# Optimization experiments

Hardware: AMD Instinct MI355X
Metric: run time of the kernel (lower is better)

Reference implementation:

```python
import jax, jax.numpy as jnp
import numpy as np

B, T, D, H = 4, 1024, 1024, 16
TP = 1024
HD = D // H
LN_EPS = 1e-3  # keras LayerNormalization default epsilon


def snac_linear(x, wt, mt):
    # conv1dsnac: w = tanh(wt) * sigmoid(mt), shape [1, nx, nf] -> [nx, nf]
    w = (jnp.tanh(wt) * jax.nn.sigmoid(mt))[0]
    return jnp.einsum('btx,xf->btf', x, w)


def layernorm(x, gamma, beta):
    mu = jnp.mean(x, axis=-1, keepdims=True)
    var = jnp.mean(jnp.square(x - mu), axis=-1, keepdims=True)
    return (x - mu) * jax.lax.rsqrt(var + LN_EPS) * gamma + beta


def setup_inputs() -> dict:
    key = jax.random.key(0)
    ks = jax.random.split(key, 10)
    s = 0.02
    return {
        'input': jax.random.normal(ks[0], (B, T, D), jnp.float32),
        'past': jax.random.normal(ks[1], (B, 2, H, TP, HD), jnp.float32),
        'qkv_wt': jax.random.normal(ks[2], (1, D, 3 * D), jnp.float32) * s,
        'qkv_mt': jax.random.normal(ks[3], (1, D, 3 * D), jnp.float32) * s,
        'merge_wt': jax.random.normal(ks[4], (1, D, D), jnp.float32) * s,
        'merge_mt': jax.random.normal(ks[5], (1, D, D), jnp.float32) * s,
        'ln1_wt': jax.random.normal(ks[6], (1, D, D), jnp.float32) * s,
        'ln1_mt': jax.random.normal(ks[7], (1, D, D), jnp.float32) * s,
        'g1': jnp.ones((D,), jnp.float32), 'b1': jnp.zeros((D,), jnp.float32),
        'g2': jnp.ones((D,), jnp.float32), 'b2': jnp.zeros((D,), jnp.float32),
    }


def reference(input, past, qkv_wt, qkv_mt, merge_wt, merge_mt, ln1_wt, ln1_mt, g1, b1, g2, b2):
    x = input
    xn = layernorm(x, g1, b1)
    c = snac_linear(xn, qkv_wt, qkv_mt)  # [B, T, 3D]
    q, k, v = jnp.split(c, 3, axis=2)
    # split heads -> [B, H, T, HD]
    to_heads = lambda t: t.reshape(B, T, H, HD).transpose(0, 2, 1, 3)
    q, k, v = to_heads(q), to_heads(k), to_heads(v)
    present = jnp.stack([k, v], axis=1)  # [B, 2, H, T, HD]
    pk, pv = past[:, 0], past[:, 1]
    k = jnp.concatenate([pk, k], axis=2)  # [B, H, TP+T, HD]
    v = jnp.concatenate([pv, v], axis=2)
    nd, ns = T, TP + T
    w = jnp.einsum('bhqd,bhkd->bhqk', q, k) * jax.lax.rsqrt(jnp.float32(HD))
    i = jnp.arange(nd)[:, None]
    j = jnp.arange(ns)[None, :]
    m = (i >= j - ns + nd).astype(w.dtype)  # [nd, ns] causal mask incl. past
    w = w * m - jnp.asarray(1e10, w.dtype) * (1 - m)
    msk = jax.nn.softmax(w, axis=-1)  # [B, H, T, TP+T]
    a = jnp.einsum('bhqk,bhkd->bhqd', msk, v)
    ah = a.transpose(0, 2, 1, 3).reshape(B, T, D)  # merge heads
    am = snac_linear(ah, merge_wt, merge_mt)
    xa = x + am
    mlp = snac_linear(layernorm(xa, g2, b2), ln1_wt, ln1_mt)
    xm = xa + mlp
    return xm, present, msk
```

## Files before the change

kernel.cpp:

```cpp
#include <hip/hip_runtime.h>
#include <hip/hip_bf16.h>

typedef _Float16 half8 __attribute__((ext_vector_type(8)));
typedef _Float16 half4v __attribute__((ext_vector_type(4)));
typedef float f32x4 __attribute__((ext_vector_type(4)));

#define DEV static __device__ __forceinline__


typedef __attribute__((address_space(1))) const unsigned int* gas_p;
typedef __attribute__((address_space(3))) unsigned int* las_p;
DEV void glds16(const void* g, void* s) {
  __builtin_amdgcn_global_load_lds((gas_p)g, (las_p)s, 16, 0, 0);
}

__global__ __launch_bounds__(256) void prep_w(const float* __restrict__ wt,
                                              const float* __restrict__ mt,
                                              _Float16* __restrict__ out, int N) {
  __shared__ float tile[64][65];
  const int ntiles = N >> 6;
  const int nt = blockIdx.x % ntiles, kt = blockIdx.x / ntiles;
  const int k0 = kt << 6, n0 = nt << 6;
  const int t = threadIdx.x, r = t >> 2, c0 = (t & 3) << 4;
  const long ibase = (long)(k0 + r) * N + n0 + c0;
#pragma unroll
  for (int j = 0; j < 16; j += 4) {
    float4 a = *(const float4*)(wt + ibase + j);
    float4 b = *(const float4*)(mt + ibase + j);
    tile[r][c0 + j + 0] = tanhf(a.x) / (1.f + __expf(-b.x));
    tile[r][c0 + j + 1] = tanhf(a.y) / (1.f + __expf(-b.y));
    tile[r][c0 + j + 2] = tanhf(a.z) / (1.f + __expf(-b.z));
    tile[r][c0 + j + 3] = tanhf(a.w) / (1.f + __expf(-b.w));
  }
  __syncthreads();
  half8 o0, o1;
#pragma unroll
  for (int j = 0; j < 8; ++j) {
    o0[j] = (_Float16)tile[c0 + j][r];
    o1[j] = (_Float16)tile[c0 + 8 + j][r];
  }
  _Float16* dst = out + (long)(n0 + r) * 1024 + k0 + c0;
  *(half8*)dst = o0;
  *(half8*)(dst + 8) = o1;
}

__global__ __launch_bounds__(256) void conv_pastk(const float* __restrict__ past,
                                                  _Float16* __restrict__ kf) {
  const long e = ((long)blockIdx.x * 256 + threadIdx.x) * 4;
  const int b = (int)(e >> 20);
  const int rem = (int)(e & 1048575);
  float4 v = *(const float4*)(past + (long)b * 2097152 + rem);
  half4v o = {(_Float16)v.x, (_Float16)v.y, (_Float16)v.z, (_Float16)v.w};
  const int h = rem >> 16, td = rem & 65535;
  *(half4v*)(kf + (long)(b * 16 + h) * 131072 + td) = o;
}

__global__ __launch_bounds__(256) void ln_k(const float* __restrict__ x,
                                            const float* __restrict__ g,
                                            const float* __restrict__ be,
                                            _Float16* __restrict__ out) {
  __shared__ float red[4];
  const int row = blockIdx.x, tid = threadIdx.x, l = tid & 63, w = tid >> 6;
  float4 v = *(const float4*)(x + (long)row * 1024 + tid * 4);
  float s = v.x + v.y + v.z + v.w;
#pragma unroll
  for (int o = 32; o > 0; o >>= 1) s += __shfl_down(s, o, 64);
  if (l == 0) red[w] = s;
  __syncthreads();
  const float mu = (red[0] + red[1] + red[2] + red[3]) * (1.f / 1024.f);
  float dx = v.x - mu, dy = v.y - mu, dz = v.z - mu, dw = v.w - mu;
  float ss = dx * dx + dy * dy + dz * dz + dw * dw;
#pragma unroll
  for (int o = 32; o > 0; o >>= 1) ss += __shfl_down(ss, o, 64);
  __syncthreads();
  if (l == 0) red[w] = ss;
  __syncthreads();
  const float var = (red[0] + red[1] + red[2] + red[3]) * (1.f / 1024.f);
  const float rs = rsqrtf(var + 1e-3f);
  float4 gv = *(const float4*)(g + tid * 4);
  float4 bv = *(const float4*)(be + tid * 4);
  half4v o = {(_Float16)(dx * rs * gv.x + bv.x), (_Float16)(dy * rs * gv.y + bv.y),
              (_Float16)(dz * rs * gv.z + bv.z), (_Float16)(dw * rs * gv.w + bv.w)};
  *(half4v*)(out + (long)row * 1024 + tid * 4) = o;
}

template <int BM, int EPI>
__global__ __launch_bounds__(256) void gemm_k(const _Float16* __restrict__ A,
                                              const _Float16* __restrict__ Bt,
                                              int mtiles,
                                              _Float16* __restrict__ e_q,
                                              _Float16* __restrict__ e_k,
                                              _Float16* __restrict__ e_v,
                                              float* __restrict__ e_present,
                                              const float* __restrict__ e_res,
                                              float* __restrict__ e_out) {
  constexpr int FM = BM / 32;
  __shared__ __align__(16) char smem[2 * BM * 128 + 32768];
  char* Bbase = smem + 2 * BM * 128;
  const int tid = threadIdx.x, l = tid & 63, w = tid >> 6;
  const int wm = w >> 1, wn = w & 1;
  const int bm = blockIdx.x % mtiles, bn = blockIdx.x / mtiles;
  const long m0 = (long)bm * BM, n0 = (long)bn * 128;

  f32x4 acc[FM][4];
#pragma unroll
  for (int i = 0; i < FM; ++i)
#pragma unroll
    for (int j = 0; j < 4; ++j) acc[i][j] = (f32x4){0.f, 0.f, 0.f, 0.f};

  auto stage = [&](int b, int kt) {
#pragma unroll
    for (int i = 0; i < FM; ++i) {
      const int cid = i * 256 + tid, row = cid >> 3, u = cid & 7;
      glds16(A + (m0 + row) * 1024 + kt * 64 + ((u ^ (row & 7)) << 3),
             smem + b * BM * 128 + i * 4096 + w * 1024);
    }
#pragma unroll
    for (int i = 0; i < 4; ++i) {
      const int cid = i * 256 + tid, row = cid >> 3, u = cid & 7;
      glds16(Bt + (n0 + row) * 1024 + kt * 64 + ((u ^ (row & 7)) << 3),
             Bbase + b * 16384 + i * 4096 + w * 1024);
    }
  };

  stage(0, 0);
  __syncthreads();
  for (int kt = 0; kt < 16; ++kt) {
    const int cur = kt & 1;
    if (kt < 15) stage(cur ^ 1, kt + 1);
    const char* As = smem + cur * BM * 128;
    const char* Bs = Bbase + cur * 16384;
#pragma unroll
    for (int k2 = 0; k2 < 2; ++k2) {
      const int sl = k2 * 4 + (l >> 4);
      half8 bfr[4];
#pragma unroll
      for (int fn = 0; fn < 4; ++fn) {
        const int rn = wn * 64 + fn * 16 + (l & 15);
        bfr[fn] = *(const half8*)(Bs + rn * 128 + ((sl ^ (rn & 7)) << 4));
      }
#pragma unroll
      for (int fm = 0; fm < FM; ++fm) {
        const int rm = wm * (BM / 2) + fm * 16 + (l & 15);
        const half8 afr = *(const half8*)(As + rm * 128 + ((sl ^ (rm & 7)) << 4));
#pragma unroll
        for (int fn = 0; fn < 4; ++fn)
          acc[fm][fn] = __builtin_amdgcn_mfma_f32_16x16x32_f16(afr, bfr[fn], acc[fm][fn], 0, 0, 0);
      }
    }
    __syncthreads();
  }
#pragma unroll
  for (int fm = 0; fm < FM; ++fm) {
#pragma unroll
    for (int fn = 0; fn < 4; ++fn) {
#pragma unroll
      for (int r = 0; r < 4; ++r) {
        const long row = m0 + wm * (BM / 2) + fm * 16 + (l >> 4) * 4 + r;
        const long col = n0 + fn * 16 + (l & 15) + wn * 64;
        const float v = acc[fm][fn][r];
        if constexpr (EPI == 0) {
          const int b = (int)(row >> 10), t = (int)(row & 1023);
          const int sec = (int)(col >> 10), h = ((int)col >> 6) & 15, hd = (int)col & 63;
          const long bh = b * 16 + h;
          if (sec == 0) {
            e_q[(bh * 1024 + t) * 64 + hd] = (_Float16)v;
          } else if (sec == 1) {
            e_present[(((long)(b * 2) * 16 + h) * 1024 + t) * 64 + hd] = v;
            e_k[(bh * 2048 + 1024 + t) * 64 + hd] = (_Float16)v;
          } else {
            e_present[(((long)(b * 2 + 1) * 16 + h) * 1024 + t) * 64 + hd] = v;
            e_v[(bh * 1024 + t) * 64 + hd] = (_Float16)v;
          }
        } else {
          e_out[row * 1024 + col] = e_res[row * 1024 + col] + v;
        }
      }
    }
  }
}

__global__ __launch_bounds__(256) void vt_transpose(const float* __restrict__ past,
                                                    const _Float16* __restrict__ vnew,
                                                    _Float16* __restrict__ vt) {
  __shared__ float tile[64][65];
  const int bh = blockIdx.x >> 5, kt = blockIdx.x & 31;
  const int b = bh >> 4, h = bh & 15;
  const int k0 = kt << 6;
  const int t = threadIdx.x, r = t >> 2, c0 = (t & 3) << 4;
  if (k0 < 1024) {
    const float* src = past + (((long)(b * 2 + 1) * 16 + h) * 1024 + (k0 + r)) * 64 + c0;
#pragma unroll
    for (int j = 0; j < 16; j += 4) {
      float4 v = *(const float4*)(src + j);
      tile[r][c0 + j + 0] = v.x;
      tile[r][c0 + j + 1] = v.y;
      tile[r][c0 + j + 2] = v.z;
      tile[r][c0 + j + 3] = v.w;
    }
  } else {
    const _Float16* src = vnew + ((long)bh * 1024 + (k0 - 1024 + r)) * 64 + c0;
    half8 a = *(const half8*)src;
    half8 bq = *(const half8*)(src + 8);
#pragma unroll
    for (int j = 0; j < 8; ++j) {
      tile[r][c0 + j] = (float)a[j];
      tile[r][c0 + 8 + j] = (float)bq[j];
    }
  }
  __syncthreads();
  half8 o0, o1;
#pragma unroll
  for (int j = 0; j < 8; ++j) {
    o0[j] = (_Float16)tile[c0 + j][r];
    o1[j] = (_Float16)tile[c0 + 8 + j][r];
  }
  _Float16* dst = vt + ((long)bh * 64 + r) * 2048 + k0 + c0;
  *(half8*)dst = o0;
  *(half8*)(dst + 8) = o1;
}

__global__ __launch_bounds__(256, 2) void attn_k(const _Float16* __restrict__ qg,
                                                 const _Float16* __restrict__ kg,
                                                 const _Float16* __restrict__ vtg,
                                                 float* __restrict__ msk,
                                                 _Float16* __restrict__ ah) {
  __shared__ __align__(16) char smem[81920];
  char* ps_all = smem + 65536;
  const int tid = threadIdx.x, l = tid & 63, w = tid >> 6;
  char* psw = ps_all + w * 4096;
  const int lq = l & 15, hi = l >> 4;

  const int x = blockIdx.x & 7, g = blockIdx.x >> 3;
  const int bh = (g & 7) * 8 + x;
  const int qt = 15 - (g >> 3);
  const int r0 = qt << 6;
  const int nc = (r0 + 1215) >> 7;
  const int rowg0 = r0 + w * 16;

  const _Float16* kb = kg + (long)bh * 131072;
  const _Float16* vb = vtg + (long)bh * 131072;
  float* mskb = msk + ((long)bh * 1024 + rowg0) * 2048;

  half8 qa[2];
  {
    const _Float16* qp = qg + ((long)bh * 1024 + rowg0 + lq) * 64 + hi * 8;
    qa[0] = *(const half8*)qp;
    qa[1] = *(const half8*)(qp + 32);
  }

  auto stageK = [&](int b, int c) {
#pragma unroll
    for (int i = 0; i < 4; ++i) {
      const int cid = i * 256 + tid, row = cid >> 3, u = cid & 7;
      glds16(kb + (long)(c * 128 + row) * 64 + ((u ^ (row & 7)) << 3),
             smem + b * 32768 + i * 4096 + w * 1024);
    }
  };
  auto stageV = [&](int b, int c) {
#pragma unroll
    for (int i = 0; i < 4; ++i) {
      const int cid = i * 256 + tid, row = cid >> 4, u = cid & 15;
      glds16(vb + (long)row * 2048 + c * 128 + ((u ^ (row & 7)) << 3),
             smem + b * 32768 + 16384 + i * 4096 + w * 1024);
    }
  };

  constexpr float C1 = 0.125f * 1.44269504088896341f;

  auto qk_tile = [&](const char* ks, f32x4 (&sa)[8]) {
#pragma unroll
    for (int fn = 0; fn < 8; ++fn) sa[fn] = (f32x4){0.f, 0.f, 0.f, 0.f};
#pragma unroll
    for (int k2 = 0; k2 < 2; ++k2) {
      const int sl = k2 * 4 + hi;
      half8 ak[8];
#pragma unroll
      for (int fn = 0; fn < 8; ++fn) {
        const int rn = fn * 16 + lq;
        ak[fn] = *(const half8*)(ks + rn * 128 + ((sl ^ (rn & 7)) << 4));
      }
#pragma unroll
      for (int fn = 0; fn < 8; ++fn)
        sa[fn] = __builtin_amdgcn_mfma_f32_16x16x32_f16(ak[fn], qa[k2], sa[fn], 0, 0, 0);
    }
  };

  const int lim = rowg0 + lq + 1024;

  float rsum = 0.f;
  stageK(0, 0);
  __syncthreads();
  for (int c = 0; c < nc; ++c) {
    const int cur = c & 1;
    if (c + 1 < nc) stageK(cur ^ 1, c + 1);
    f32x4 sa[8];
    qk_tile(smem + cur * 32768, sa);
    if (c < nc - 1) {
#pragma unroll
      for (int fn = 0; fn < 8; ++fn)
#pragma unroll
        for (int r = 0; r < 4; ++r) rsum += __builtin_amdgcn_exp2f(sa[fn][r] * C1);
    } else {
#pragma unroll
      for (int fn = 0; fn < 8; ++fn)
#pragma unroll
        for (int r = 0; r < 4; ++r) {
          const int col = c * 128 + fn * 16 + hi * 4 + r;
          const float e = __builtin_amdgcn_exp2f(sa[fn][r] * C1);
          rsum += (col <= lim) ? e : 0.f;
        }
    }
    __syncthreads();
  }
  rsum += __shfl_xor(rsum, 16, 64);
  rsum += __shfl_xor(rsum, 32, 64);
  const float c2s = -__builtin_amdgcn_logf(rsum);

  f32x4 pv[4];
#pragma unroll
  for (int j = 0; j < 4; ++j) pv[j] = (f32x4){0.f, 0.f, 0.f, 0.f};
  stageK(0, 0);
  stageV(0, 0);
  __syncthreads();
  for (int c = 0; c < nc; ++c) {
    const int cur = c & 1;
    if (c + 1 < nc) {
      stageK(cur ^ 1, c + 1);
      stageV(cur ^ 1, c + 1);
    }
    f32x4 sa[8];
    qk_tile(smem + cur * 32768, sa);
    const bool bound = (c == nc - 1);
#pragma unroll
    for (int fn = 0; fn < 8; ++fn) {
      float pr[4];
#pragma unroll
      for (int r = 0; r < 4; ++r) {
        float p = __builtin_amdgcn_exp2f(sa[fn][r] * C1 + c2s);
        if (bound) {
          const int col = c * 128 + fn * 16 + hi * 4 + r;
          p = (col <= lim) ? p : 0.f;
        }
        pr[r] = p;
      }
      *(float4*)(mskb + (long)lq * 2048 + c * 128 + fn * 16 + hi * 4) =
          make_float4(pr[0], pr[1], pr[2], pr[3]);
      const half4v hv = {(_Float16)pr[0], (_Float16)pr[1], (_Float16)pr[2],
                         (_Float16)pr[3]};
      const int bc = fn * 32 + hi * 8;
      *(half4v*)(psw + lq * 256 + ((((bc >> 4) ^ (lq & 7)) << 4) | (bc & 15))) = hv;
    }
    __builtin_amdgcn_wave_barrier();
    asm volatile("s_waitcnt lgkmcnt(0)" ::: "memory");
    __builtin_amdgcn_sched_barrier(0);
    const char* vs = smem + cur * 32768 + 16384;
#pragma unroll
    for (int k2p = 0; k2p < 4; ++k2p) {
      const int sl2 = k2p * 4 + hi;
      const half8 pa = *(const half8*)(psw + lq * 256 + ((sl2 ^ (lq & 7)) << 4));
      half8 bv[4];
#pragma unroll
      for (int fn2 = 0; fn2 < 4; ++fn2) {
        const int rd = fn2 * 16 + lq;
        bv[fn2] = *(const half8*)(vs + rd * 256 + ((sl2 ^ (rd & 7)) << 4));
      }
#pragma unroll
      for (int fn2 = 0; fn2 < 4; ++fn2)
        pv[fn2] = __builtin_amdgcn_mfma_f32_16x16x32_f16(pa, bv[fn2], pv[fn2], 0, 0, 0);
    }
    __syncthreads();
  }

  const int ntail = (16 - nc) << 5;
  if (ntail > 0) {
    const float4 z4 = make_float4(0.f, 0.f, 0.f, 0.f);
    for (int row = 0; row < 16; ++row)
      for (int i = l; i < ntail; i += 64)
        *(float4*)(mskb + (long)row * 2048 + nc * 128 + i * 4) = z4;
  }

  const int b_ = bh >> 4, h_ = bh & 15;
  _Float16* ahb = ah + ((long)b_ * 1024 + rowg0) * 1024 + h_ * 64;
#pragma unroll
  for (int fn2 = 0; fn2 < 4; ++fn2)
#pragma unroll
    for (int r = 0; r < 4; ++r)
      ahb[(long)(hi * 4 + r) * 1024 + fn2 * 16 + lq] = (_Float16)pv[fn2][r];
}

extern "C" void kernel_launch(void* const* d_in, const int* in_sizes, int n_in,
                              void* d_out, int out_size, void* d_ws, size_t ws_size,
                              hipStream_t stream) {
  const float* x = (const float*)d_in[0];
  const float* past = (const float*)d_in[1];
  const float* qkv_wt = (const float*)d_in[2];
  const float* qkv_mt = (const float*)d_in[3];
  const float* merge_wt = (const float*)d_in[4];
  const float* merge_mt = (const float*)d_in[5];
  const float* ln1_wt = (const float*)d_in[6];
  const float* ln1_mt = (const float*)d_in[7];
  const float* g1 = (const float*)d_in[8];
  const float* b1 = (const float*)d_in[9];
  const float* g2 = (const float*)d_in[10];
  const float* b2 = (const float*)d_in[11];

  float* out = (float*)d_out;
  float* o_xm = out;
  float* o_present = out + 4194304;
  float* o_msk = out + 4194304 + 8388608;

  char* ws = (char*)d_ws;
  _Float16* wq_t = (_Float16*)(ws + 0);
  _Float16* wm_t = (_Float16*)(ws + 6291456);
  _Float16* wl_t = (_Float16*)(ws + 8388608);
  _Float16* xn   = (_Float16*)(ws + 10485760);
  _Float16* qws  = (_Float16*)(ws + 18874368);
  _Float16* kful = (_Float16*)(ws + 27262976);
  _Float16* vnew = (_Float16*)(ws + 44040192);
  _Float16* vt   = (_Float16*)(ws + 52428800);
  _Float16* ah   = (_Float16*)(ws + 69206016);
  float* xa      = (float*)(ws + 77594624);

  prep_w<<<768, 256, 0, stream>>>(qkv_wt, qkv_mt, wq_t, 3072);
  prep_w<<<256, 256, 0, stream>>>(merge_wt, merge_mt, wm_t, 1024);
  prep_w<<<256, 256, 0, stream>>>(ln1_wt, ln1_mt, wl_t, 1024);
  conv_pastk<<<4096, 256, 0, stream>>>(past, kful);
  ln_k<<<4096, 256, 0, stream>>>(x, g1, b1, xn);
  gemm_k<128, 0><<<768, 256, 0, stream>>>(xn, wq_t, 32, qws, kful, vnew, o_present,
                                          nullptr, nullptr);
  vt_transpose<<<2048, 256, 0, stream>>>(past, vnew, vt);
  attn_k<<<1024, 256, 0, stream>>>(qws, kful, vt, o_msk, ah);
  gemm_k<64, 1><<<512, 256, 0, stream>>>(ah, wm_t, 64, nullptr, nullptr, nullptr,
                                         nullptr, x, xa);
  ln_k<<<4096, 256, 0, stream>>>(xa, g2, b2, xn);
  gemm_k<64, 1><<<512, 256, 0, stream>>>(xn, wl_t, 64, nullptr, nullptr, nullptr,
                                         nullptr, xa, o_xm);
}
```

Before: 302.7 us.

## Read K and V directly from global, shrink LDS, raise occupancy, nontemporal mask stores

The first softmax-denominator pass now loads K fragments straight from global memory into registers instead of staging them through double-buffered LDS with block barriers. The second pass no longer stages V in LDS and reads V^T fragments directly from global. Together these cut LDS use from 80KB to 48KB so launch bounds can request 3 blocks per CU. The large fp32 mask output is written with nontemporal stores to avoid polluting cache. The trade-off is more uncoalesced global and L2 traffic for K and V and higher register pressure under the tighter occupancy bound.

```diff
diff --git a/kernel.cpp b/kernel.cpp
--- a/kernel.cpp
+++ b/kernel.cpp
@@ -12,6 +12,9 @@
 typedef __attribute__((address_space(3))) unsigned int* las_p;
 DEV void glds16(const void* g, void* s) {
   __builtin_amdgcn_global_load_lds((gas_p)g, (las_p)s, 16, 0, 0);
+}
+DEV void nt_store4(float* p, f32x4 v) {
+  __builtin_nontemporal_store(v, (f32x4*)p);
 }
 
 __global__ __launch_bounds__(256) void prep_w(const float* __restrict__ wt,
@@ -220,13 +223,13 @@
   *(half8*)(dst + 8) = o1;
 }
 
-__global__ __launch_bounds__(256, 2) void attn_k(const _Float16* __restrict__ qg,
+__global__ __launch_bounds__(256, 3) void attn_k(const _Float16* __restrict__ qg,
                                                  const _Float16* __restrict__ kg,
                                                  const _Float16* __restrict__ vtg,
                                                  float* __restrict__ msk,
                                                  _Float16* __restrict__ ah) {
-  __shared__ __align__(16) char smem[81920];
-  char* ps_all = smem + 65536;
+  __shared__ __align__(16) char smem[49152];
+  char* ps_all = smem + 32768;
   const int tid = threadIdx.x, l = tid & 63, w = tid >> 6;
   char* psw = ps_all + w * 4096;
   const int lq = l & 15, hi = l >> 4;
@@ -254,48 +257,30 @@
     for (int i = 0; i < 4; ++i) {
       const int cid = i * 256 + tid, row = cid >> 3, u = cid & 7;
       glds16(kb + (long)(c * 128 + row) * 64 + ((u ^ (row & 7)) << 3),
-             smem + b * 32768 + i * 4096 + w * 1024);
+             smem + b * 16384 + i * 4096 + w * 1024);
     }
   };
-  auto stageV = [&](int b, int c) {
-#pragma unroll
-    for (int i = 0; i < 4; ++i) {
-      const int cid = i * 256 + tid, row = cid >> 4, u = cid & 15;
-      glds16(vb + (long)row * 2048 + c * 128 + ((u ^ (row & 7)) << 3),
-             smem + b * 32768 + 16384 + i * 4096 + w * 1024);
-    }
-  };
 
   constexpr float C1 = 0.125f * 1.44269504088896341f;
-
-  auto qk_tile = [&](const char* ks, f32x4 (&sa)[8]) {
+  const int lim = rowg0 + lq + 1024;
+
+  float rsum = 0.f;
+  for (int c = 0; c < nc; ++c) {
+    half8 ak[2][8];
+#pragma unroll
+    for (int k2 = 0; k2 < 2; ++k2)
+#pragma unroll
+      for (int fn = 0; fn < 8; ++fn)
+        ak[k2][fn] = *(const half8*)(kb + (long)(c * 128 + fn * 16 + lq) * 64 +
+                                     k2 * 32 + hi * 8);
+    f32x4 sa[8];
 #pragma unroll
     for (int fn = 0; fn < 8; ++fn) sa[fn] = (f32x4){0.f, 0.f, 0.f, 0.f};
 #pragma unroll
-    for (int k2 = 0; k2 < 2; ++k2) {
-      const int sl = k2 * 4 + hi;
-      half8 ak[8];
-#pragma unroll
-      for (int fn = 0; fn < 8; ++fn) {
-        const int rn = fn * 16 + lq;
-        ak[fn] = *(const half8*)(ks + rn * 128 + ((sl ^ (rn & 7)) << 4));
-      }
+    for (int k2 = 0; k2 < 2; ++k2)
 #pragma unroll
       for (int fn = 0; fn < 8; ++fn)
-        sa[fn] = __builtin_amdgcn_mfma_f32_16x16x32_f16(ak[fn], qa[k2], sa[fn], 0, 0, 0);
-    }
-  };
-
-  const int lim = rowg0 + lq + 1024;
-
-  float rsum = 0.f;
-  stageK(0, 0);
-  __syncthreads();
-  for (int c = 0; c < nc; ++c) {
-    const int cur = c & 1;
-    if (c + 1 < nc) stageK(cur ^ 1, c + 1);
-    f32x4 sa[8];
-    qk_tile(smem + cur * 32768, sa);
+        sa[fn] = __builtin_amdgcn_mfma_f32_16x16x32_f16(ak[k2][fn], qa[k2], sa[fn], 0, 0, 0);
     if (c < nc - 1) {
 #pragma unroll
       for (int fn = 0; fn < 8; ++fn)
@@ -311,26 +296,39 @@
           rsum += (col <= lim) ? e : 0.f;
         }
     }
-    __syncthreads();
   }
   rsum += __shfl_xor(rsum, 16, 64);
   rsum += __shfl_xor(rsum, 32, 64);
   const float c2s = -__builtin_amdgcn_logf(rsum);
 
+  auto qk_tile = [&](const char* ks, f32x4 (&sa)[8]) {
+#pragma unroll
+    for (int fn = 0; fn < 8; ++fn) sa[fn] = (f32x4){0.f, 0.f, 0.f, 0.f};
+#pragma unroll
+    for (int k2 = 0; k2 < 2; ++k2) {
+      const int sl = k2 * 4 + hi;
+      half8 ak[8];
+#pragma unroll
+      for (int fn = 0; fn < 8; ++fn) {
+        const int rn = fn * 16 + lq;
+        ak[fn] = *(const half8*)(ks + rn * 128 + ((sl ^ (rn & 7)) << 4));
+      }
+#pragma unroll
+      for (int fn = 0; fn < 8; ++fn)
+        sa[fn] = __builtin_amdgcn_mfma_f32_16x16x32_f16(ak[fn], qa[k2], sa[fn], 0, 0, 0);
+    }
+  };
+
   f32x4 pv[4];
 #pragma unroll
   for (int j = 0; j < 4; ++j) pv[j] = (f32x4){0.f, 0.f, 0.f, 0.f};
   stageK(0, 0);
-  stageV(0, 0);
   __syncthreads();
   for (int c = 0; c < nc; ++c) {
     const int cur = c & 1;
-    if (c + 1 < nc) {
-      stageK(cur ^ 1, c + 1);
-      stageV(cur ^ 1, c + 1);
-    }
+    if (c + 1 < nc) stageK(cur ^ 1, c + 1);
     f32x4 sa[8];
-    qk_tile(smem + cur * 32768, sa);
+    qk_tile(smem + cur * 16384, sa);
     const bool bound = (c == nc - 1);
 #pragma unroll
     for (int fn = 0; fn < 8; ++fn) {
@@ -344,8 +342,8 @@
         }
         pr[r] = p;
       }
-      *(float4*)(mskb + (long)lq * 2048 + c * 128 + fn * 16 + hi * 4) =
-          make_float4(pr[0], pr[1], pr[2], pr[3]);
+      nt_store4(mskb + (long)lq * 2048 + c * 128 + fn * 16 + hi * 4,
+                (f32x4){pr[0], pr[1], pr[2], pr[3]});
       const half4v hv = {(_Float16)pr[0], (_Float16)pr[1], (_Float16)pr[2],
                          (_Float16)pr[3]};
       const int bc = fn * 32 + hi * 8;
@@ -354,17 +352,14 @@
     __builtin_amdgcn_wave_barrier();
     asm volatile("s_waitcnt lgkmcnt(0)" ::: "memory");
     __builtin_amdgcn_sched_barrier(0);
-    const char* vs = smem + cur * 32768 + 16384;
 #pragma unroll
     for (int k2p = 0; k2p < 4; ++k2p) {
       const int sl2 = k2p * 4 + hi;
       const half8 pa = *(const half8*)(psw + lq * 256 + ((sl2 ^ (lq & 7)) << 4));
       half8 bv[4];
 #pragma unroll
-      for (int fn2 = 0; fn2 < 4; ++fn2) {
-        const int rd = fn2 * 16 + lq;
-        bv[fn2] = *(const half8*)(vs + rd * 256 + ((sl2 ^ (rd & 7)) << 4));
-      }
+      for (int fn2 = 0; fn2 < 4; ++fn2)
+        bv[fn2] = *(const half8*)(vb + (long)(fn2 * 16 + lq) * 2048 + c * 128 + sl2 * 8);
 #pragma unroll
       for (int fn2 = 0; fn2 < 4; ++fn2)
         pv[fn2] = __builtin_amdgcn_mfma_f32_16x16x32_f16(pa, bv[fn2], pv[fn2], 0, 0, 0);
@@ -374,10 +369,10 @@
 
   const int ntail = (16 - nc) << 5;
   if (ntail > 0) {
-    const float4 z4 = make_float4(0.f, 0.f, 0.f, 0.f);
     for (int row = 0; row < 16; ++row)
       for (int i = l; i < ntail; i += 64)
-        *(float4*)(mskb + (long)row * 2048 + nc * 128 + i * 4) = z4;
+        nt_store4(mskb + (long)row * 2048 + nc * 128 + i * 4,
+                  (f32x4){0.f, 0.f, 0.f, 0.f});
   }
 
   const int b_ = bh >> 4, h_ = bh & 15;
```

New measurement: 352.2 us. 16.4% more time.

## Shrink attention KV chunk to 64 for higher occupancy and merge prep launches

Applied to the files above, without the earlier changes.

The attention kernel now processes keys in 64-column chunks instead of 128, cutting shared memory from 80KB to 40KB and raising launch bounds to 4 blocks per CU, so more waves can hide latency. In exchange there are twice as many loop iterations and barriers. The three weight-prep launches are merged into one kernel, and the past-K conversion is merged with the V transpose into one launch, which reduces launch count. The K conversion now runs after the QKV GEMM, which also writes new K rows into the same kful buffer; the two writes cover disjoint regions.

```diff
diff --git a/kernel.cpp b/kernel.cpp
--- a/kernel.cpp
+++ b/kernel.cpp
@@ -14,12 +14,28 @@
   __builtin_amdgcn_global_load_lds((gas_p)g, (las_p)s, 16, 0, 0);
 }
 
-__global__ __launch_bounds__(256) void prep_w(const float* __restrict__ wt,
-                                              const float* __restrict__ mt,
-                                              _Float16* __restrict__ out, int N) {
+__global__ __launch_bounds__(256) void prep_all(const float* __restrict__ qkv_wt,
+                                                const float* __restrict__ qkv_mt,
+                                                const float* __restrict__ mg_wt,
+                                                const float* __restrict__ mg_mt,
+                                                const float* __restrict__ l1_wt,
+                                                const float* __restrict__ l1_mt,
+                                                _Float16* __restrict__ wq,
+                                                _Float16* __restrict__ wm,
+                                                _Float16* __restrict__ wl) {
   __shared__ float tile[64][65];
+  const float *wt, *mt;
+  _Float16* out;
+  int N, bid;
+  if (blockIdx.x < 768) {
+    wt = qkv_wt; mt = qkv_mt; out = wq; N = 3072; bid = blockIdx.x;
+  } else if (blockIdx.x < 1024) {
+    wt = mg_wt; mt = mg_mt; out = wm; N = 1024; bid = blockIdx.x - 768;
+  } else {
+    wt = l1_wt; mt = l1_mt; out = wl; N = 1024; bid = blockIdx.x - 1024;
+  }
   const int ntiles = N >> 6;
-  const int nt = blockIdx.x % ntiles, kt = blockIdx.x / ntiles;
+  const int nt = bid % ntiles, kt = bid / ntiles;
   const int k0 = kt << 6, n0 = nt << 6;
   const int t = threadIdx.x, r = t >> 2, c0 = (t & 3) << 4;
   const long ibase = (long)(k0 + r) * N + n0 + c0;
@@ -44,15 +60,56 @@
   *(half8*)(dst + 8) = o1;
 }
 
-__global__ __launch_bounds__(256) void conv_pastk(const float* __restrict__ past,
-                                                  _Float16* __restrict__ kf) {
-  const long e = ((long)blockIdx.x * 256 + threadIdx.x) * 4;
-  const int b = (int)(e >> 20);
-  const int rem = (int)(e & 1048575);
-  float4 v = *(const float4*)(past + (long)b * 2097152 + rem);
-  half4v o = {(_Float16)v.x, (_Float16)v.y, (_Float16)v.z, (_Float16)v.w};
-  const int h = rem >> 16, td = rem & 65535;
-  *(half4v*)(kf + (long)(b * 16 + h) * 131072 + td) = o;
+__global__ __launch_bounds__(256) void kv_prep(const float* __restrict__ past,
+                                               const _Float16* __restrict__ vnew,
+                                               _Float16* __restrict__ kf,
+                                               _Float16* __restrict__ vt) {
+  __shared__ float tile[64][65];
+  if (blockIdx.x < 4096) {
+    const long e = ((long)blockIdx.x * 256 + threadIdx.x) * 4;
+    const int b = (int)(e >> 20);
+    const int rem = (int)(e & 1048575);
+    float4 v = *(const float4*)(past + (long)b * 2097152 + rem);
+    half4v o = {(_Float16)v.x, (_Float16)v.y, (_Float16)v.z, (_Float16)v.w};
+    const int h = rem >> 16, td = rem & 65535;
+    *(half4v*)(kf + (long)(b * 16 + h) * 131072 + td) = o;
+    return;
+  }
+  const int bid = blockIdx.x - 4096;
+  const int bh = bid >> 5, kt = bid & 31;
+  const int b = bh >> 4, h = bh & 15;
+  const int k0 = kt << 6;
+  const int t = threadIdx.x, r = t >> 2, c0 = (t & 3) << 4;
+  if (k0 < 1024) {
+    const float* src = past + (((long)(b * 2 + 1) * 16 + h) * 1024 + (k0 + r)) * 64 + c0;
+#pragma unroll
+    for (int j = 0; j < 16; j += 4) {
+      float4 v = *(const float4*)(src + j);
+      tile[r][c0 + j + 0] = v.x;
+      tile[r][c0 + j + 1] = v.y;
+      tile[r][c0 + j + 2] = v.z;
+      tile[r][c0 + j + 3] = v.w;
+    }
+  } else {
+    const _Float16* src = vnew + ((long)bh * 1024 + (k0 - 1024 + r)) * 64 + c0;
+    half8 a = *(const half8*)src;
+    half8 bq = *(const half8*)(src + 8);
+#pragma unroll
+    for (int j = 0; j < 8; ++j) {
+      tile[r][c0 + j] = (float)a[j];
+      tile[r][c0 + 8 + j] = (float)bq[j];
+    }
+  }
+  __syncthreads();
+  half8 o0, o1;
+#pragma unroll
+  for (int j = 0; j < 8; ++j) {
+    o0[j] = (_Float16)tile[c0 + j][r];
+    o1[j] = (_Float16)tile[c0 + 8 + j][r];
+  }
+  _Float16* dst = vt + ((long)bh * 64 + r) * 2048 + k0 + c0;
+  *(half8*)dst = o0;
+  *(half8*)(dst + 8) = o1;
 }
 
 __global__ __launch_bounds__(256) void ln_k(const float* __restrict__ x,
@@ -180,62 +237,22 @@
   }
 }
 
-__global__ __launch_bounds__(256) void vt_transpose(const float* __restrict__ past,
-                                                    const _Float16* __restrict__ vnew,
-                                                    _Float16* __restrict__ vt) {
-  __shared__ float tile[64][65];
-  const int bh = blockIdx.x >> 5, kt = blockIdx.x & 31;
-  const int b = bh >> 4, h = bh & 15;
-  const int k0 = kt << 6;
-  const int t = threadIdx.x, r = t >> 2, c0 = (t & 3) << 4;
-  if (k0 < 1024) {
-    const float* src = past + (((long)(b * 2 + 1) * 16 + h) * 1024 + (k0 + r)) * 64 + c0;
-#pragma unroll
-    for (int j = 0; j < 16; j += 4) {
-      float4 v = *(const float4*)(src + j);
-      tile[r][c0 + j + 0] = v.x;
-      tile[r][c0 + j + 1] = v.y;
-      tile[r][c0 + j + 2] = v.z;
-      tile[r][c0 + j + 3] = v.w;
-    }
-  } else {
-    const _Float16* src = vnew + ((long)bh * 1024 + (k0 - 1024 + r)) * 64 + c0;
-    half8 a = *(const half8*)src;
-    half8 bq = *(const half8*)(src + 8);
-#pragma unroll
-    for (int j = 0; j < 8; ++j) {
-      tile[r][c0 + j] = (float)a[j];
-      tile[r][c0 + 8 + j] = (float)bq[j];
-    }
-  }
-  __syncthreads();
-  half8 o0, o1;
-#pragma unroll
-  for (int j = 0; j < 8; ++j) {
-    o0[j] = (_Float16)tile[c0 + j][r];
-    o1[j] = (_Float16)tile[c0 + 8 + j][r];
-  }
-  _Float16* dst = vt + ((long)bh * 64 + r) * 2048 + k0 + c0;
-  *(half8*)dst = o0;
-  *(half8*)(dst + 8) = o1;
-}
-
-__global__ __launch_bounds__(256, 2) void attn_k(const _Float16* __restrict__ qg,
+__global__ __launch_bounds__(256, 4) void attn_k(const _Float16* __restrict__ qg,
                                                  const _Float16* __restrict__ kg,
                                                  const _Float16* __restrict__ vtg,
                                                  float* __restrict__ msk,
                                                  _Float16* __restrict__ ah) {
-  __shared__ __align__(16) char smem[81920];
-  char* ps_all = smem + 65536;
+  __shared__ __align__(16) char smem[40960];
+  char* ps_all = smem + 32768;
   const int tid = threadIdx.x, l = tid & 63, w = tid >> 6;
-  char* psw = ps_all + w * 4096;
+  char* psw = ps_all + w * 2048;
   const int lq = l & 15, hi = l >> 4;
 
   const int x = blockIdx.x & 7, g = blockIdx.x >> 3;
   const int bh = (g & 7) * 8 + x;
   const int qt = 15 - (g >> 3);
   const int r0 = qt << 6;
-  const int nc = (r0 + 1215) >> 7;
+  const int nc = (r0 + 1151) >> 6;
   const int rowg0 = r0 + w * 16;
 
   const _Float16* kb = kg + (long)bh * 131072;
@@ -251,42 +268,41 @@
 
   auto stageK = [&](int b, int c) {
 #pragma unroll
-    for (int i = 0; i < 4; ++i) {
+    for (int i = 0; i < 2; ++i) {
       const int cid = i * 256 + tid, row = cid >> 3, u = cid & 7;
-      glds16(kb + (long)(c * 128 + row) * 64 + ((u ^ (row & 7)) << 3),
-             smem + b * 32768 + i * 4096 + w * 1024);
+      glds16(kb + (long)(c * 64 + row) * 64 + ((u ^ (row & 7)) << 3),
+             smem + b * 8192 + i * 4096 + w * 1024);
     }
   };
   auto stageV = [&](int b, int c) {
 #pragma unroll
-    for (int i = 0; i < 4; ++i) {
-      const int cid = i * 256 + tid, row = cid >> 4, u = cid & 15;
-      glds16(vb + (long)row * 2048 + c * 128 + ((u ^ (row & 7)) << 3),
-             smem + b * 32768 + 16384 + i * 4096 + w * 1024);
+    for (int i = 0; i < 2; ++i) {
+      const int cid = i * 256 + tid, row = cid >> 3, u = cid & 7;
+      glds16(vb + (long)row * 2048 + c * 64 + ((u ^ (row & 7)) << 3),
+             smem + 16384 + b * 8192 + i * 4096 + w * 1024);
     }
   };
 
   constexpr float C1 = 0.125f * 1.44269504088896341f;
-
-  auto qk_tile = [&](const char* ks, f32x4 (&sa)[8]) {
-#pragma unroll
-    for (int fn = 0; fn < 8; ++fn) sa[fn] = (f32x4){0.f, 0.f, 0.f, 0.f};
+  const int lim = rowg0 + lq + 1024;
+
+  auto qk_tile = [&](const char* ks, f32x4 (&sa)[4]) {
+#pragma unroll
+    for (int fn = 0; fn < 4; ++fn) sa[fn] = (f32x4){0.f, 0.f, 0.f, 0.f};
 #pragma unroll
     for (int k2 = 0; k2 < 2; ++k2) {
       const int sl = k2 * 4 + hi;
-      half8 ak[8];
-#pragma unroll
-      for (int fn = 0; fn < 8; ++fn) {
+      half8 ak[4];
+#pragma unroll
+      for (int fn = 0; fn < 4; ++fn) {
         const int rn = fn * 16 + lq;
         ak[fn] = *(const half8*)(ks + rn * 128 + ((sl ^ (rn & 7)) << 4));
       }
 #pragma unroll
-      for (int fn = 0; fn < 8; ++fn)
+      for (int fn = 0; fn < 4; ++fn)
         sa[fn] = __builtin_amdgcn_mfma_f32_16x16x32_f16(ak[fn], qa[k2], sa[fn], 0, 0, 0);
     }
   };
-
-  const int lim = rowg0 + lq + 1024;
 
   float rsum = 0.f;
   stageK(0, 0);
@@ -294,19 +310,19 @@
   for (int c = 0; c < nc; ++c) {
     const int cur = c & 1;
     if (c + 1 < nc) stageK(cur ^ 1, c + 1);
-    f32x4 sa[8];
-    qk_tile(smem + cur * 32768, sa);
+    f32x4 sa[4];
+    qk_tile(smem + cur * 8192, sa);
     if (c < nc - 1) {
 #pragma unroll
-      for (int fn = 0; fn < 8; ++fn)
+      for (int fn = 0; fn < 4; ++fn)
 #pragma unroll
         for (int r = 0; r < 4; ++r) rsum += __builtin_amdgcn_exp2f(sa[fn][r] * C1);
     } else {
 #pragma unroll
-      for (int fn = 0; fn < 8; ++fn)
+      for (int fn = 0; fn < 4; ++fn)
 #pragma unroll
         for (int r = 0; r < 4; ++r) {
-          const int col = c * 128 + fn * 16 + hi * 4 + r;
+          const int col = c * 64 + fn * 16 + hi * 4 + r;
           const float e = __builtin_amdgcn_exp2f(sa[fn][r] * C1);
           rsum += (col <= lim) ? e : 0.f;
         }
@@ -329,41 +345,41 @@
       stageK(cur ^ 1, c + 1);
       stageV(cur ^ 1, c + 1);
     }
-    f32x4 sa[8];
-    qk_tile(smem + cur * 32768, sa);
+    f32x4 sa[4];
+    qk_tile(smem + cur * 8192, sa);
     const bool bound = (c == nc - 1);
 #pragma unroll
-    for (int fn = 0; fn < 8; ++fn) {
+    for (int fn = 0; fn < 4; ++fn) {
       float pr[4];
 #pragma unroll
       for (int r = 0; r < 4; ++r) {
         float p = __builtin_amdgcn_exp2f(sa[fn][r] * C1 + c2s);
         if (bound) {
-          const int col = c * 128 + fn * 16 + hi * 4 + r;
+          const int col = c * 64 + fn * 16 + hi * 4 + r;
           p = (col <= lim) ? p : 0.f;
         }
         pr[r] = p;
       }
-      *(float4*)(mskb + (long)lq * 2048 + c * 128 + fn * 16 + hi * 4) =
+      *(float4*)(mskb + (long)lq * 2048 + c * 64 + fn * 16 + hi * 4) =
           make_float4(pr[0], pr[1], pr[2], pr[3]);
       const half4v hv = {(_Float16)pr[0], (_Float16)pr[1], (_Float16)pr[2],
                          (_Float16)pr[3]};
       const int bc = fn * 32 + hi * 8;
-      *(half4v*)(psw + lq * 256 + ((((bc >> 4) ^ (lq & 7)) << 4) | (bc & 15))) = hv;
+      *(half4v*)(psw + lq * 128 + ((((bc >> 4) ^ (lq & 7)) << 4) | (bc & 15))) = hv;
     }
     __builtin_amdgcn_wave_barrier();
     asm volatile("s_waitcnt lgkmcnt(0)" ::: "memory");
     __builtin_amdgcn_sched_barrier(0);
-    const char* vs = smem + cur * 32768 + 16384;
-#pragma unroll
-    for (int k2p = 0; k2p < 4; ++k2p) {
+    const char* vs = smem + 16384 + cur * 8192;
+#pragma unroll
+    for (int k2p = 0; k2p < 2; ++k2p) {
       const int sl2 = k2p * 4 + hi;
-      const half8 pa = *(const half8*)(psw + lq * 256 + ((sl2 ^ (lq & 7)) << 4));
+      const half8 pa = *(const half8*)(psw + lq * 128 + ((sl2 ^ (lq & 7)) << 4));
       half8 bv[4];
 #pragma unroll
       for (int fn2 = 0; fn2 < 4; ++fn2) {
         const int rd = fn2 * 16 + lq;
-        bv[fn2] = *(const half8*)(vs + rd * 256 + ((sl2 ^ (rd & 7)) << 4));
+        bv[fn2] = *(const half8*)(vs + rd * 128 + ((sl2 ^ (rd & 7)) << 4));
       }
 #pragma unroll
       for (int fn2 = 0; fn2 < 4; ++fn2)
@@ -372,12 +388,12 @@
     __syncthreads();
   }
 
-  const int ntail = (16 - nc) << 5;
+  const int ntail = 512 - (nc << 4);
   if (ntail > 0) {
     const float4 z4 = make_float4(0.f, 0.f, 0.f, 0.f);
     for (int row = 0; row < 16; ++row)
       for (int i = l; i < ntail; i += 64)
-        *(float4*)(mskb + (long)row * 2048 + nc * 128 + i * 4) = z4;
+        *(float4*)(mskb + (long)row * 2048 + nc * 64 + i * 4) = z4;
   }
 
   const int b_ = bh >> 4, h_ = bh & 15;
@@ -422,14 +438,12 @@
   _Float16* ah   = (_Float16*)(ws + 69206016);
   float* xa      = (float*)(ws + 77594624);
 
-  prep_w<<<768, 256, 0, stream>>>(qkv_wt, qkv_mt, wq_t, 3072);
-  prep_w<<<256, 256, 0, stream>>>(merge_wt, merge_mt, wm_t, 1024);
-  prep_w<<<256, 256, 0, stream>>>(ln1_wt, ln1_mt, wl_t, 1024);
-  conv_pastk<<<4096, 256, 0, stream>>>(past, kful);
+  prep_all<<<1280, 256, 0, stream>>>(qkv_wt, qkv_mt, merge_wt, merge_mt, ln1_wt,
+                                     ln1_mt, wq_t, wm_t, wl_t);
   ln_k<<<4096, 256, 0, stream>>>(x, g1, b1, xn);
   gemm_k<128, 0><<<768, 256, 0, stream>>>(xn, wq_t, 32, qws, kful, vnew, o_present,
                                           nullptr, nullptr);
-  vt_transpose<<<2048, 256, 0, stream>>>(past, vnew, vt);
+  kv_prep<<<6144, 256, 0, stream>>>(past, vnew, kful, vt);
   attn_k<<<1024, 256, 0, stream>>>(qws, kful, vt, o_msk, ah);
   gemm_k<64, 1><<<512, 256, 0, stream>>>(ah, wm_t, 64, nullptr, nullptr, nullptr,
                                          nullptr, x, xa);
```

Result: no change. 308.1 us (+1.8%).
